# Optimization experiments

Hardware: AMD Instinct MI355X
Metric: run time of the kernel (lower is better)

The kernel has to match this reference:

```python
import jax, jax.numpy as jnp
import numpy as np

H = 512        # edge_feature_size (input_size == hidden_size)
B = 8          # batch
N = 8192       # n_nodes


def setup_inputs() -> dict:
    key = jax.random.key(0)
    k1, k2, k3, k4 = jax.random.split(key, 4)
    # Glorot-ish init scale like torch GRU (uniform +-1/sqrt(H))
    s = 1.0 / np.sqrt(H)
    e_wv = jax.random.normal(k1, (B, H, N), dtype=jnp.float32)
    m_wv = jax.random.normal(k2, (B, H, N), dtype=jnp.float32)
    # torch GRU weight layout: [3H, H] stacked as (reset, update, new)
    W_ih = jax.random.uniform(k3, (3 * H, H), dtype=jnp.float32, minval=-s, maxval=s)
    W_hh = jax.random.uniform(k4, (3 * H, H), dtype=jnp.float32, minval=-s, maxval=s)
    return {"e_wv": e_wv, "m_wv": m_wv, "W_ih": W_ih, "W_hh": W_hh}


def reference(e_wv, m_wv, W_ih, W_hh):
    # Single-step GRU cell (no bias), applied to all nodes at once.
    # e_wv: hidden state h0 [B, H, N]; m_wv: input x [B, H, N].
    gi = jnp.einsum('gh,bhn->bgn', W_ih, m_wv)   # [B, 3H, N]
    gh = jnp.einsum('gh,bhn->bgn', W_hh, e_wv)   # [B, 3H, N]
    i_r, i_z, i_n = gi[:, :H], gi[:, H:2 * H], gi[:, 2 * H:]
    h_r, h_z, h_n = gh[:, :H], gh[:, H:2 * H], gh[:, 2 * H:]
    r = jax.nn.sigmoid(i_r + h_r)
    z = jax.nn.sigmoid(i_z + h_z)
    n = jnp.tanh(i_n + r * h_n)
    return (1.0 - z) * n + z * e_wv              # [B, H, N]
```

## Files before the change

kernel.cpp:

```cpp
#include <hip/hip_runtime.h>
#include <hip/hip_bf16.h>


#define HH 512
#define NBATCH 8
#define NN 8192
#define BN 128
#define BK 64
#define NSTEPS 16
#define THREADS 256
#define A_BYTES (192 * BK * 2)
#define B_BYTES (BN * BK * 2)
#define BUF_BYTES (A_BYTES + B_BYTES)
#define LDS_TOTAL (2 * BUF_BYTES)

typedef __attribute__((ext_vector_type(8))) short short8;
typedef __attribute__((ext_vector_type(4))) float f32x4;

__device__ __forceinline__ unsigned cvt_pk_bf16(float a, float b) {
  unsigned r;
  asm("v_cvt_pk_bf16_f32 %0, %1, %2" : "=v"(r) : "v"(a), "v"(b));
  return r;
}

__device__ __forceinline__ void gload_lds16(const void* g, void* l) {
  __builtin_amdgcn_global_load_lds(
      (__attribute__((address_space(1))) void*)(g),
      (__attribute__((address_space(3))) void*)(l), 16, 0, 0);
}

#define MFMA16(a_, b_, c_) __builtin_amdgcn_mfma_f32_16x16x32_bf16((a_), (b_), (c_), 0, 0, 0)

__global__ void prepack_w(const float* __restrict__ W_ih, const float* __restrict__ W_hh,
                          __hip_bfloat16* __restrict__ ws) {
  int t = blockIdx.x * 256 + threadIdx.x;
  int blk = t / 12288;
  int e = t % 12288;
  int ra = e >> 6;
  int kk = (e & 63) ^ ((ra & 7) << 3);
  int gate = ra >> 6;
  int h = (blk >> 4) * 64 + (ra & 63);
  int row = gate * HH + h;
  int kg = (blk & 15) * 64 + kk;
  float v = (kg < 512) ? W_ih[row * 512 + kg] : W_hh[row * 512 + (kg - 512)];
  ws[t] = __float2bfloat16(v);
}

__global__ __launch_bounds__(THREADS, 2)
void gru_main(const float* __restrict__ e_wv, const float* __restrict__ m_wv,
              const __hip_bfloat16* __restrict__ wimg, float* __restrict__ out) {
  extern __shared__ char smem[];
  const int tid  = threadIdx.x;
  const int lane = tid & 63;
  const int wave = tid >> 6;
  const int wm = wave >> 1;
  const int wn = wave & 1;

  const int wg  = blockIdx.x;
  const int swz = (wg & 7) * 512 + (wg >> 3);
  const int ht  = swz & 7;
  const int nt  = (swz >> 3) & 63;
  const int b   = swz >> 9;

  const int k0  = (tid & 15) << 2;
  const int n0s = (tid >> 4) << 3;

  const size_t batch_off = (size_t)b * HH * NN;
  const float* xm = m_wv + batch_off + (size_t)k0 * NN + nt * BN + n0s;
  const float* xe = e_wv + batch_off + (size_t)k0 * NN + nt * BN + n0s;
  const char*  wA = (const char*)wimg + (size_t)ht * NSTEPS * A_BYTES + tid * 16;

  f32x4 acc_r[2][4]  = {};
  f32x4 acc_z[2][4]  = {};
  f32x4 acc_in[2][4] = {};
  f32x4 acc_hn[2][4] = {};

  int aoff[2], boff[2];
#pragma unroll
  for (int kb2 = 0; kb2 < 2; ++kb2) {
    const int ke2 = kb2 * 64 + ((lane >> 4) << 4);
    const int sw  = (lane & 7) << 4;
    aoff[kb2] = (wm * 32 + (lane & 15)) * 128 + (ke2 ^ sw);
    boff[kb2] = A_BYTES + (wn * 64 + (lane & 15)) * 128 + (ke2 ^ sw);
  }

  auto issue_A = [&](int s, char* nb) {
    const char* gA = wA + (size_t)s * A_BYTES;
    char* lA = nb + tid * 16;
#pragma unroll
    for (int i = 0; i < 6; ++i)
      gload_lds16(gA + i * 4096, lA + i * 4096);
  };
  auto x_load_half = [&](const float* xs, int h, f32x4 c[4]) {
#pragma unroll
    for (int i = 0; i < 4; ++i) c[i] = *(const f32x4*)(xs + (size_t)i * NN + h * 4);
  };
  auto x_write_half = [&](char* nb, int h, const f32x4 c[4]) {
    char* Bb = nb + A_BYTES;
#pragma unroll
    for (int j2 = 0; j2 < 4; ++j2) {
      const int j = h * 4 + j2;
      unsigned lo = cvt_pk_bf16(c[0][j2], c[1][j2]);
      unsigned hi = cvt_pk_bf16(c[2][j2], c[3][j2]);
      int off = (n0s + j) * 128 + ((k0 * 2) ^ (j << 4));
      *(uint2*)(Bb + off) = make_uint2(lo, hi);
    }
  };
  auto compute_kb2 = [&](const char* cb, int kb2, bool firstHalf) {
    short8 bfr[4];
#pragma unroll
    for (int ni = 0; ni < 4; ++ni)
      bfr[ni] = *(const short8*)(cb + boff[kb2] + ni * 2048);
    {
      short8 a0 = *(const short8*)(cb + aoff[kb2]);
      short8 a1 = *(const short8*)(cb + aoff[kb2] + 2048);
#pragma unroll
      for (int ni = 0; ni < 4; ++ni) {
        acc_r[0][ni] = MFMA16(a0, bfr[ni], acc_r[0][ni]);
        acc_r[1][ni] = MFMA16(a1, bfr[ni], acc_r[1][ni]);
      }
    }
    {
      short8 a0 = *(const short8*)(cb + aoff[kb2] + 8192);
      short8 a1 = *(const short8*)(cb + aoff[kb2] + 8192 + 2048);
#pragma unroll
      for (int ni = 0; ni < 4; ++ni) {
        acc_z[0][ni] = MFMA16(a0, bfr[ni], acc_z[0][ni]);
        acc_z[1][ni] = MFMA16(a1, bfr[ni], acc_z[1][ni]);
      }
    }
    {
      short8 a0 = *(const short8*)(cb + aoff[kb2] + 16384);
      short8 a1 = *(const short8*)(cb + aoff[kb2] + 16384 + 2048);
      if (firstHalf) {
#pragma unroll
        for (int ni = 0; ni < 4; ++ni) {
          acc_in[0][ni] = MFMA16(a0, bfr[ni], acc_in[0][ni]);
          acc_in[1][ni] = MFMA16(a1, bfr[ni], acc_in[1][ni]);
        }
      } else {
#pragma unroll
        for (int ni = 0; ni < 4; ++ni) {
          acc_hn[0][ni] = MFMA16(a0, bfr[ni], acc_hn[0][ni]);
          acc_hn[1][ni] = MFMA16(a1, bfr[ni], acc_hn[1][ni]);
        }
      }
    }
  };

  issue_A(0, smem);
  {
    f32x4 c[4];
    x_load_half(xm, 0, c);
    x_write_half(smem, 0, c);
    x_load_half(xm, 1, c);
    x_write_half(smem, 1, c);
  }
  __syncthreads();

#pragma unroll 1
  for (int s = 0; s < NSTEPS; ++s) {
    char* cb = smem + ((s & 1) ? BUF_BYTES : 0);
    char* nb = smem + ((s & 1) ? 0 : BUF_BYTES);
    const bool pre = (s < NSTEPS - 1);
    const bool firstHalf = (s < 8);
    const float* xs = (s + 1 < 8 ? xm : xe) + (size_t)((s + 1) & 7) * (64 * NN);

    f32x4 c[4];
    if (pre) x_load_half(xs, 0, c);
    if (pre) issue_A(s + 1, nb);
    compute_kb2(cb, 0, firstHalf);
    if (pre) { x_write_half(nb, 0, c); x_load_half(xs, 1, c); }
    compute_kb2(cb, 1, firstHalf);
    if (pre) x_write_half(nb, 1, c);
    __syncthreads();
  }

  const size_t obase = batch_off + (size_t)(ht * 64 + wm * 32) * NN + nt * BN + wn * 64;
  const float* ep = e_wv + obase;
  float* op = out + obase;
  const int rsub = (lane >> 4) << 2;
  const int csub = lane & 15;
#pragma unroll
  for (int mi = 0; mi < 2; ++mi)
#pragma unroll
    for (int ni = 0; ni < 4; ++ni) {
#pragma unroll
      for (int r = 0; r < 4; ++r) {
        size_t idx = (size_t)(mi * 16 + rsub + r) * NN + ni * 16 + csub;
        float pr  = acc_r[mi][ni][r];
        float pz  = acc_z[mi][ni][r];
        float vin = acc_in[mi][ni][r];
        float vhn = acc_hn[mi][ni][r];
        float rr  = 1.f / (1.f + __expf(-pr));
        float zz  = 1.f / (1.f + __expf(-pz));
        float ex  = __expf(2.f * (vin + rr * vhn));
        float nn2 = 1.f - 2.f / (ex + 1.f);
        float ev  = ep[idx];
        op[idx] = (1.f - zz) * nn2 + zz * ev;
      }
    }
}

extern "C" void kernel_launch(void* const* d_in, const int* in_sizes, int n_in,
                              void* d_out, int out_size, void* d_ws, size_t ws_size,
                              hipStream_t stream) {
  const float* e_wv = (const float*)d_in[0];
  const float* m_wv = (const float*)d_in[1];
  const float* W_ih = (const float*)d_in[2];
  const float* W_hh = (const float*)d_in[3];
  float* out = (float*)d_out;
  __hip_bfloat16* wimg = (__hip_bfloat16*)d_ws;

  (void)hipFuncSetAttribute((const void*)gru_main,
                            hipFuncAttributeMaxDynamicSharedMemorySize, LDS_TOTAL);

  prepack_w<<<(NBATCH * NSTEPS * 12288) / 256, 256, 0, stream>>>(W_ih, W_hh, wimg);
  gru_main<<<NBATCH * 8 * 64, THREADS, LDS_TOTAL, stream>>>(e_wv, m_wv, wimg, out);
}
```

Baseline: 385.0 us.

## Deepen X prefetch to two stages ahead and raise MFMA wave priority

Activation tiles are now loaded from global memory two K-steps ahead into registers and converted to bf16 after the MFMA block. The packed values are written to LDS at the start of the next step, before the weight async copy is issued. The MFMA compute section is also wrapped in s_setprio to favour matrix issue. The aim is to hide global load latency behind a full step of compute. In exchange the live registers rise (cA, cB, pk), which may pressure occupancy at two blocks per SIMD.

Measured after the change: 373.1 us. 3.1% less time.

```diff
diff --git a/kernel.cpp b/kernel.cpp
--- a/kernel.cpp
+++ b/kernel.cpp
@@ -75,6 +75,9 @@
   f32x4 acc_in[2][4] = {};
   f32x4 acc_hn[2][4] = {};
 
+  f32x4 cA[4], cB[4];
+  uint2 pk[8];
+
   int aoff[2], boff[2];
 #pragma unroll
   for (int kb2 = 0; kb2 < 2; ++kb2) {
@@ -91,19 +94,28 @@
     for (int i = 0; i < 6; ++i)
       gload_lds16(gA + i * 4096, lA + i * 4096);
   };
-  auto x_load_half = [&](const float* xs, int h, f32x4 c[4]) {
-#pragma unroll
-    for (int i = 0; i < 4; ++i) c[i] = *(const f32x4*)(xs + (size_t)i * NN + h * 4);
-  };
-  auto x_write_half = [&](char* nb, int h, const f32x4 c[4]) {
+  auto x_load = [&](const float* xs) {
+#pragma unroll
+    for (int i = 0; i < 4; ++i) {
+      cA[i] = *(const f32x4*)(xs + (size_t)i * NN);
+      cB[i] = *(const f32x4*)(xs + (size_t)i * NN + 4);
+    }
+  };
+  auto x_cvt = [&]() {
+#pragma unroll
+    for (int j = 0; j < 4; ++j) {
+      pk[j]     = make_uint2(cvt_pk_bf16(cA[0][j], cA[1][j]),
+                             cvt_pk_bf16(cA[2][j], cA[3][j]));
+      pk[j + 4] = make_uint2(cvt_pk_bf16(cB[0][j], cB[1][j]),
+                             cvt_pk_bf16(cB[2][j], cB[3][j]));
+    }
+  };
+  auto write_X = [&](char* nb) {
     char* Bb = nb + A_BYTES;
 #pragma unroll
-    for (int j2 = 0; j2 < 4; ++j2) {
-      const int j = h * 4 + j2;
-      unsigned lo = cvt_pk_bf16(c[0][j2], c[1][j2]);
-      unsigned hi = cvt_pk_bf16(c[2][j2], c[3][j2]);
+    for (int j = 0; j < 8; ++j) {
       int off = (n0s + j) * 128 + ((k0 * 2) ^ (j << 4));
-      *(uint2*)(Bb + off) = make_uint2(lo, hi);
+      *(uint2*)(Bb + off) = pk[j];
     }
   };
   auto compute_kb2 = [&](const char* cb, int kb2, bool firstHalf) {
@@ -149,30 +161,32 @@
   };
 
   issue_A(0, smem);
-  {
-    f32x4 c[4];
-    x_load_half(xm, 0, c);
-    x_write_half(smem, 0, c);
-    x_load_half(xm, 1, c);
-    x_write_half(smem, 1, c);
-  }
+  x_load(xm);
+  x_cvt();
+  write_X(smem);
+  x_load(xm + (size_t)(64 * NN));
+  x_cvt();
   __syncthreads();
 
 #pragma unroll 1
   for (int s = 0; s < NSTEPS; ++s) {
     char* cb = smem + ((s & 1) ? BUF_BYTES : 0);
     char* nb = smem + ((s & 1) ? 0 : BUF_BYTES);
-    const bool pre = (s < NSTEPS - 1);
     const bool firstHalf = (s < 8);
-    const float* xs = (s + 1 < 8 ? xm : xe) + (size_t)((s + 1) & 7) * (64 * NN);
-
-    f32x4 c[4];
-    if (pre) x_load_half(xs, 0, c);
-    if (pre) issue_A(s + 1, nb);
+
+    if (s < NSTEPS - 2) {
+      const int t = s + 2;
+      x_load((t < 8 ? xm : xe) + (size_t)(t & 7) * (64 * NN));
+    }
+    if (s < NSTEPS - 1) {
+      write_X(nb);
+      issue_A(s + 1, nb);
+    }
+    __builtin_amdgcn_s_setprio(1);
     compute_kb2(cb, 0, firstHalf);
-    if (pre) { x_write_half(nb, 0, c); x_load_half(xs, 1, c); }
     compute_kb2(cb, 1, firstHalf);
-    if (pre) x_write_half(nb, 1, c);
+    __builtin_amdgcn_s_setprio(0);
+    if (s < NSTEPS - 2) x_cvt();
     __syncthreads();
   }
 
```

## Prefetch weights and inputs into registers two steps ahead, drop direct LDS loads

Applied to the files above, without the earlier changes.

Replaces the direct global-to-LDS weight loads and the split half-tile input loads with a register-staged pipeline. Weights and input rows for step s+2 are loaded into registers while step s computes, then written to LDS after the MFMA block. The input load mapping is also changed so each wave loads contiguous float2 columns per row, and the MFMA section runs at raised wave priority with a lighter barrier that waits only on LDS. This is meant to hide global latency more deeply, at the cost of extra VGPRs (6 uint4 plus 16 float2) that may hurt occupancy at two blocks per CU.

After: 633.9 us. 64.6% more time.

```diff
diff --git a/kernel.cpp b/kernel.cpp
--- a/kernel.cpp
+++ b/kernel.cpp
@@ -23,13 +23,14 @@
   return r;
 }
 
-__device__ __forceinline__ void gload_lds16(const void* g, void* l) {
-  __builtin_amdgcn_global_load_lds(
-      (__attribute__((address_space(1))) void*)(g),
-      (__attribute__((address_space(3))) void*)(l), 16, 0, 0);
-}
-
 #define MFMA16(a_, b_, c_) __builtin_amdgcn_mfma_f32_16x16x32_bf16((a_), (b_), (c_), 0, 0, 0)
+
+#define WG_BARRIER() do {                                   \
+    asm volatile("s_waitcnt lgkmcnt(0)" ::: "memory");      \
+    __builtin_amdgcn_sched_barrier(0);                      \
+    __builtin_amdgcn_s_barrier();                           \
+    __builtin_amdgcn_sched_barrier(0);                      \
+  } while (0)
 
 __global__ void prepack_w(const float* __restrict__ W_ih, const float* __restrict__ W_hh,
                           __hip_bfloat16* __restrict__ ws) {
@@ -55,6 +56,7 @@
   const int wave = tid >> 6;
   const int wm = wave >> 1;
   const int wn = wave & 1;
+  const int KW = wave << 4;
 
   const int wg  = blockIdx.x;
   const int swz = (wg & 7) * 512 + (wg >> 3);
@@ -62,18 +64,18 @@
   const int nt  = (swz >> 3) & 63;
   const int b   = swz >> 9;
 
-  const int k0  = (tid & 15) << 2;
-  const int n0s = (tid >> 4) << 3;
-
   const size_t batch_off = (size_t)b * HH * NN;
-  const float* xm = m_wv + batch_off + (size_t)k0 * NN + nt * BN + n0s;
-  const float* xe = e_wv + batch_off + (size_t)k0 * NN + nt * BN + n0s;
+  const float* xm = m_wv + batch_off + (size_t)KW * NN + nt * BN + 2 * lane;
+  const float* xe = e_wv + batch_off + (size_t)KW * NN + nt * BN + 2 * lane;
   const char*  wA = (const char*)wimg + (size_t)ht * NSTEPS * A_BYTES + tid * 16;
 
   f32x4 acc_r[2][4]  = {};
   f32x4 acc_z[2][4]  = {};
   f32x4 acc_in[2][4] = {};
   f32x4 acc_hn[2][4] = {};
+
+  uint4  aR[6];
+  float2 xR[16];
 
   int aoff[2], boff[2];
 #pragma unroll
@@ -84,28 +86,39 @@
     boff[kb2] = A_BYTES + (wn * 64 + (lane & 15)) * 128 + (ke2 ^ sw);
   }
 
-  auto issue_A = [&](int s, char* nb) {
-    const char* gA = wA + (size_t)s * A_BYTES;
+  auto issue_AX = [&](int t) {
+    const char* gA = wA + (size_t)t * A_BYTES;
+#pragma unroll
+    for (int i = 0; i < 6; ++i)
+      aR[i] = *(const uint4*)(gA + i * 4096);
+    const float* xs = (t < 8 ? xm : xe) + (size_t)(t & 7) * (64 * NN);
+#pragma unroll
+    for (int g = 0; g < 4; ++g)
+#pragma unroll
+      for (int u = 0; u < 4; ++u)
+        xR[g * 4 + u] = *(const float2*)(xs + (size_t)(g * 4 + u) * NN);
+  };
+
+  auto write_AX = [&](char* nb) {
     char* lA = nb + tid * 16;
 #pragma unroll
     for (int i = 0; i < 6; ++i)
-      gload_lds16(gA + i * 4096, lA + i * 4096);
+      *(uint4*)(lA + i * 4096) = aR[i];
+    char* Bb = nb + A_BYTES;
+    const int n0 = 2 * lane;
+#pragma unroll
+    for (int g = 0; g < 4; ++g) {
+      uint2 w0, w1;
+      w0.x = cvt_pk_bf16(xR[g * 4 + 0].x, xR[g * 4 + 1].x);
+      w0.y = cvt_pk_bf16(xR[g * 4 + 2].x, xR[g * 4 + 3].x);
+      w1.x = cvt_pk_bf16(xR[g * 4 + 0].y, xR[g * 4 + 1].y);
+      w1.y = cvt_pk_bf16(xR[g * 4 + 2].y, xR[g * 4 + 3].y);
+      const int kb = (KW + g * 4) * 2;
+      *(uint2*)(Bb + n0 * 128 + (kb ^ ((n0 & 7) << 4)))            = w0;
+      *(uint2*)(Bb + (n0 + 1) * 128 + (kb ^ (((n0 + 1) & 7) << 4))) = w1;
+    }
   };
-  auto x_load_half = [&](const float* xs, int h, f32x4 c[4]) {
-#pragma unroll
-    for (int i = 0; i < 4; ++i) c[i] = *(const f32x4*)(xs + (size_t)i * NN + h * 4);
-  };
-  auto x_write_half = [&](char* nb, int h, const f32x4 c[4]) {
-    char* Bb = nb + A_BYTES;
-#pragma unroll
-    for (int j2 = 0; j2 < 4; ++j2) {
-      const int j = h * 4 + j2;
-      unsigned lo = cvt_pk_bf16(c[0][j2], c[1][j2]);
-      unsigned hi = cvt_pk_bf16(c[2][j2], c[3][j2]);
-      int off = (n0s + j) * 128 + ((k0 * 2) ^ (j << 4));
-      *(uint2*)(Bb + off) = make_uint2(lo, hi);
-    }
-  };
+
   auto compute_kb2 = [&](const char* cb, int kb2, bool firstHalf) {
     short8 bfr[4];
 #pragma unroll
@@ -148,32 +161,27 @@
     }
   };
 
-  issue_A(0, smem);
-  {
-    f32x4 c[4];
-    x_load_half(xm, 0, c);
-    x_write_half(smem, 0, c);
-    x_load_half(xm, 1, c);
-    x_write_half(smem, 1, c);
-  }
-  __syncthreads();
+  issue_AX(0);
+  write_AX(smem);
+  issue_AX(1);
+  WG_BARRIER();
 
 #pragma unroll 1
   for (int s = 0; s < NSTEPS; ++s) {
     char* cb = smem + ((s & 1) ? BUF_BYTES : 0);
     char* nb = smem + ((s & 1) ? 0 : BUF_BYTES);
-    const bool pre = (s < NSTEPS - 1);
     const bool firstHalf = (s < 8);
-    const float* xs = (s + 1 < 8 ? xm : xe) + (size_t)((s + 1) & 7) * (64 * NN);
-
-    f32x4 c[4];
-    if (pre) x_load_half(xs, 0, c);
-    if (pre) issue_A(s + 1, nb);
+
+    __builtin_amdgcn_s_setprio(1);
     compute_kb2(cb, 0, firstHalf);
-    if (pre) { x_write_half(nb, 0, c); x_load_half(xs, 1, c); }
     compute_kb2(cb, 1, firstHalf);
-    if (pre) x_write_half(nb, 1, c);
-    __syncthreads();
+    __builtin_amdgcn_s_setprio(0);
+
+    if (s + 1 < NSTEPS) {
+      write_AX(nb);
+      if (s + 2 < NSTEPS) issue_AX(s + 2);
+      WG_BARRIER();
+    }
   }
 
   const size_t obase = batch_off + (size_t)(ht * 64 + wm * 32) * NN + nt * BN + wn * 64;
```

## Double workgroup size to 8 waves and simplify X staging with priority hints

Applied to the files above, without the earlier changes.

Raises the block from 4 to 8 waves in a 2x4 wave grid, so each wave owns a 32x32 output tile and holds half as many accumulators. Each thread now loads and converts only four X columns, issued in one load before compute and written to LDS after compute, instead of two interleaved half-loads. s_setprio raises wave priority around the MFMA section. The aim is more latency hiding and lower register pressure, at the cost of more LDS fragment reads per MFMA and longer register lifetimes for the X data.

After: 426.3 us. +10.7%, slower.

```diff
diff --git a/kernel.cpp b/kernel.cpp
--- a/kernel.cpp
+++ b/kernel.cpp
@@ -8,7 +8,7 @@
 #define BN 128
 #define BK 64
 #define NSTEPS 16
-#define THREADS 256
+#define THREADS 512
 #define A_BYTES (192 * BK * 2)
 #define B_BYTES (BN * BK * 2)
 #define BUF_BYTES (A_BYTES + B_BYTES)
@@ -46,15 +46,15 @@
   ws[t] = __float2bfloat16(v);
 }
 
-__global__ __launch_bounds__(THREADS, 2)
+__global__ __launch_bounds__(THREADS, 4)
 void gru_main(const float* __restrict__ e_wv, const float* __restrict__ m_wv,
               const __hip_bfloat16* __restrict__ wimg, float* __restrict__ out) {
   extern __shared__ char smem[];
   const int tid  = threadIdx.x;
   const int lane = tid & 63;
   const int wave = tid >> 6;
-  const int wm = wave >> 1;
-  const int wn = wave & 1;
+  const int wm = wave >> 2;
+  const int wn = wave & 3;
 
   const int wg  = blockIdx.x;
   const int swz = (wg & 7) * 512 + (wg >> 3);
@@ -63,17 +63,18 @@
   const int b   = swz >> 9;
 
   const int k0  = (tid & 15) << 2;
-  const int n0s = (tid >> 4) << 3;
+  const int n0s = (tid >> 4) << 2;
 
   const size_t batch_off = (size_t)b * HH * NN;
   const float* xm = m_wv + batch_off + (size_t)k0 * NN + nt * BN + n0s;
   const float* xe = e_wv + batch_off + (size_t)k0 * NN + nt * BN + n0s;
   const char*  wA = (const char*)wimg + (size_t)ht * NSTEPS * A_BYTES + tid * 16;
 
-  f32x4 acc_r[2][4]  = {};
-  f32x4 acc_z[2][4]  = {};
-  f32x4 acc_in[2][4] = {};
-  f32x4 acc_hn[2][4] = {};
+  f32x4 acc_r[2][2]  = {};
+  f32x4 acc_z[2][2]  = {};
+  f32x4 acc_in[2][2] = {};
+  f32x4 acc_hn[2][2] = {};
+  f32x4 bv[4];
 
   int aoff[2], boff[2];
 #pragma unroll
@@ -81,41 +82,41 @@
     const int ke2 = kb2 * 64 + ((lane >> 4) << 4);
     const int sw  = (lane & 7) << 4;
     aoff[kb2] = (wm * 32 + (lane & 15)) * 128 + (ke2 ^ sw);
-    boff[kb2] = A_BYTES + (wn * 64 + (lane & 15)) * 128 + (ke2 ^ sw);
+    boff[kb2] = A_BYTES + (wn * 32 + (lane & 15)) * 128 + (ke2 ^ sw);
   }
 
   auto issue_A = [&](int s, char* nb) {
     const char* gA = wA + (size_t)s * A_BYTES;
     char* lA = nb + tid * 16;
-#pragma unroll
-    for (int i = 0; i < 6; ++i)
-      gload_lds16(gA + i * 4096, lA + i * 4096);
-  };
-  auto x_load_half = [&](const float* xs, int h, f32x4 c[4]) {
-#pragma unroll
-    for (int i = 0; i < 4; ++i) c[i] = *(const f32x4*)(xs + (size_t)i * NN + h * 4);
-  };
-  auto x_write_half = [&](char* nb, int h, const f32x4 c[4]) {
+    gload_lds16(gA,          lA);
+    gload_lds16(gA + 8192,   lA + 8192);
+    gload_lds16(gA + 16384,  lA + 16384);
+  };
+  auto x_load = [&](const float* xs) {
+#pragma unroll
+    for (int i = 0; i < 4; ++i) bv[i] = *(const f32x4*)(xs + (size_t)i * NN);
+  };
+  auto write_X = [&](char* nb) {
     char* Bb = nb + A_BYTES;
 #pragma unroll
-    for (int j2 = 0; j2 < 4; ++j2) {
-      const int j = h * 4 + j2;
-      unsigned lo = cvt_pk_bf16(c[0][j2], c[1][j2]);
-      unsigned hi = cvt_pk_bf16(c[2][j2], c[3][j2]);
-      int off = (n0s + j) * 128 + ((k0 * 2) ^ (j << 4));
+    for (int j = 0; j < 4; ++j) {
+      unsigned lo = cvt_pk_bf16(bv[0][j], bv[1][j]);
+      unsigned hi = cvt_pk_bf16(bv[2][j], bv[3][j]);
+      const int n = n0s + j;
+      int off = n * 128 + ((k0 * 2) ^ ((n & 7) << 4));
       *(uint2*)(Bb + off) = make_uint2(lo, hi);
     }
   };
   auto compute_kb2 = [&](const char* cb, int kb2, bool firstHalf) {
-    short8 bfr[4];
-#pragma unroll
-    for (int ni = 0; ni < 4; ++ni)
+    short8 bfr[2];
+#pragma unroll
+    for (int ni = 0; ni < 2; ++ni)
       bfr[ni] = *(const short8*)(cb + boff[kb2] + ni * 2048);
     {
       short8 a0 = *(const short8*)(cb + aoff[kb2]);
       short8 a1 = *(const short8*)(cb + aoff[kb2] + 2048);
 #pragma unroll
-      for (int ni = 0; ni < 4; ++ni) {
+      for (int ni = 0; ni < 2; ++ni) {
         acc_r[0][ni] = MFMA16(a0, bfr[ni], acc_r[0][ni]);
         acc_r[1][ni] = MFMA16(a1, bfr[ni], acc_r[1][ni]);
       }
@@ -124,7 +125,7 @@
       short8 a0 = *(const short8*)(cb + aoff[kb2] + 8192);
       short8 a1 = *(const short8*)(cb + aoff[kb2] + 8192 + 2048);
 #pragma unroll
-      for (int ni = 0; ni < 4; ++ni) {
+      for (int ni = 0; ni < 2; ++ni) {
         acc_z[0][ni] = MFMA16(a0, bfr[ni], acc_z[0][ni]);
         acc_z[1][ni] = MFMA16(a1, bfr[ni], acc_z[1][ni]);
       }
@@ -134,13 +135,13 @@
       short8 a1 = *(const short8*)(cb + aoff[kb2] + 16384 + 2048);
       if (firstHalf) {
 #pragma unroll
-        for (int ni = 0; ni < 4; ++ni) {
+        for (int ni = 0; ni < 2; ++ni) {
           acc_in[0][ni] = MFMA16(a0, bfr[ni], acc_in[0][ni]);
           acc_in[1][ni] = MFMA16(a1, bfr[ni], acc_in[1][ni]);
         }
       } else {
 #pragma unroll
-        for (int ni = 0; ni < 4; ++ni) {
+        for (int ni = 0; ni < 2; ++ni) {
           acc_hn[0][ni] = MFMA16(a0, bfr[ni], acc_hn[0][ni]);
           acc_hn[1][ni] = MFMA16(a1, bfr[ni], acc_hn[1][ni]);
         }
@@ -149,13 +150,8 @@
   };
 
   issue_A(0, smem);
-  {
-    f32x4 c[4];
-    x_load_half(xm, 0, c);
-    x_write_half(smem, 0, c);
-    x_load_half(xm, 1, c);
-    x_write_half(smem, 1, c);
-  }
+  x_load(xm);
+  write_X(smem);
   __syncthreads();
 
 #pragma unroll 1
@@ -164,19 +160,21 @@
     char* nb = smem + ((s & 1) ? 0 : BUF_BYTES);
     const bool pre = (s < NSTEPS - 1);
     const bool firstHalf = (s < 8);
-    const float* xs = (s + 1 < 8 ? xm : xe) + (size_t)((s + 1) & 7) * (64 * NN);
-
-    f32x4 c[4];
-    if (pre) x_load_half(xs, 0, c);
-    if (pre) issue_A(s + 1, nb);
+
+    if (pre) {
+      const int t = s + 1;
+      x_load((t < 8 ? xm : xe) + (size_t)(t & 7) * (64 * NN));
+      issue_A(t, nb);
+    }
+    __builtin_amdgcn_s_setprio(1);
     compute_kb2(cb, 0, firstHalf);
-    if (pre) { x_write_half(nb, 0, c); x_load_half(xs, 1, c); }
     compute_kb2(cb, 1, firstHalf);
-    if (pre) x_write_half(nb, 1, c);
+    __builtin_amdgcn_s_setprio(0);
+    if (pre) write_X(nb);
     __syncthreads();
   }
 
-  const size_t obase = batch_off + (size_t)(ht * 64 + wm * 32) * NN + nt * BN + wn * 64;
+  const size_t obase = batch_off + (size_t)(ht * 64 + wm * 32) * NN + nt * BN + wn * 32;
   const float* ep = e_wv + obase;
   float* op = out + obase;
   const int rsub = (lane >> 4) << 2;
@@ -184,7 +182,7 @@
 #pragma unroll
   for (int mi = 0; mi < 2; ++mi)
 #pragma unroll
-    for (int ni = 0; ni < 4; ++ni) {
+    for (int ni = 0; ni < 2; ++ni) {
 #pragma unroll
       for (int r = 0; r < 4; ++r) {
         size_t idx = (size_t)(mi * 16 + rsub + r) * NN + ni * 16 + csub;
```
